# Performance work log

Measured on AMD Instinct MI355X. Metric: run time of the kernel, lower is better.

## Reference

```python
import jax, jax.numpy as jnp
import numpy as np

N, DIM = 8192, 128

def setup_inputs() -> dict:
    key = jax.random.key(0)
    ks = jax.random.split(key, 9)
    s = 1.0 / np.sqrt(DIM)
    return {
        "x": jax.random.normal(ks[0], (N, DIM), dtype=jnp.float32),
        "Wq": jax.random.uniform(ks[1], (DIM, DIM), jnp.float32, -s, s),
        "bq": jax.random.uniform(ks[2], (DIM,), jnp.float32, -s, s),
        "Wk": jax.random.uniform(ks[3], (DIM, DIM), jnp.float32, -s, s),
        "bk": jax.random.uniform(ks[4], (DIM,), jnp.float32, -s, s),
        "Wv": jax.random.uniform(ks[5], (DIM, DIM), jnp.float32, -s, s),
        "bv": jax.random.uniform(ks[6], (DIM,), jnp.float32, -s, s),
        "Wo": jax.random.uniform(ks[7], (DIM, DIM), jnp.float32, -s, s),
        "bo": jax.random.uniform(ks[8], (DIM,), jnp.float32, -s, s),
    }

def reference(x, Wq, bq, Wk, bk, Wv, bv, Wo, bo):
    # nn.Linear: y = x @ W.T + b
    Q = x @ Wq.T + bq                      # [N, d]
    K = x @ Wk.T + bk                      # [N, d]
    V = x @ Wv.T + bv                      # [N, d]
    scale = 1.0 / jnp.sqrt(jnp.asarray(x.shape[-1], x.dtype))
    scores = (Q @ K.T) * scale             # [N, N] — matches original O(n^2) math
    attn = jax.nn.softmax(scores, axis=-1)
    out = attn @ V                         # [N, d]
    return out @ Wo.T + bo
```

## Files before the change

kernel.cpp:

```cpp
#include <hip/hip_runtime.h>
#include <math.h>


typedef __bf16 bf16x8 __attribute__((ext_vector_type(8)));
typedef float f32x4 __attribute__((ext_vector_type(4)));
typedef float f32x16 __attribute__((ext_vector_type(16)));
typedef unsigned int u32x4 __attribute__((ext_vector_type(4)));
typedef unsigned int u32x2 __attribute__((ext_vector_type(2)));
typedef unsigned short us16;

#define NTOK 8192
#define CHUNKS 8

static constexpr float SCALE_L2E = 0.08838834764831845f * 1.4426950408889634f;

__device__ __forceinline__ unsigned f2bf_u(float x) {
    unsigned u = __builtin_bit_cast(unsigned, x);
    return (u + 0x7FFFu + ((u >> 16) & 1u)) >> 16;
}

__device__ __forceinline__ unsigned pk_bf16(float x, float y) {
    unsigned a = __builtin_bit_cast(unsigned, x) + 0x8000u;
    unsigned b = __builtin_bit_cast(unsigned, y) + 0x8000u;
#if __has_builtin(__builtin_amdgcn_perm)
    return __builtin_amdgcn_perm(b, a, 0x07060302u);
#else
    return (a >> 16) | (b & 0xFFFF0000u);
#endif
}

__device__ __forceinline__ bf16x8 ld_frag(const us16* p) {
    u32x4 u = *reinterpret_cast<const u32x4*>(p);
    return __builtin_bit_cast(bf16x8, u);
}

__device__ __forceinline__ bf16x8 cvt_frag(const float* p) {
    f32x4 a = *reinterpret_cast<const f32x4*>(p);
    f32x4 b = *reinterpret_cast<const f32x4*>(p + 4);
    u32x4 o;
    o[0] = f2bf_u(a[0]) | (f2bf_u(a[1]) << 16);
    o[1] = f2bf_u(a[2]) | (f2bf_u(a[3]) << 16);
    o[2] = f2bf_u(b[0]) | (f2bf_u(b[1]) << 16);
    o[3] = f2bf_u(b[2]) | (f2bf_u(b[3]) << 16);
    return __builtin_bit_cast(bf16x8, o);
}

__global__ __launch_bounds__(256) void proj_qkv(
    const float* __restrict__ x,
    const float* __restrict__ wq, const float* __restrict__ bq,
    const float* __restrict__ wk, const float* __restrict__ bk,
    const float* __restrict__ wv, const float* __restrict__ bv,
    us16* __restrict__ Qb, us16* __restrict__ Kb, us16* __restrict__ Vt)
{
    __shared__ us16 ldsT[4][16 * 136];

    int z = blockIdx.x >> 7;
    int tile = blockIdx.x & 127;
    const float* W = z == 0 ? wq : z == 1 ? wk : wv;
    const float* bias = z == 0 ? bq : z == 1 ? bk : bv;
    float osc = z == 0 ? SCALE_L2E : 1.0f;

    int w = threadIdx.x >> 6, lane = threadIdx.x & 63;
    int quad = lane >> 4, l15 = lane & 15;
    int rbase = tile * 64 + w * 16;

    bf16x8 af[4];
#pragma unroll
    for (int ks = 0; ks < 4; ++ks)
        af[ks] = cvt_frag(x + (rbase + l15) * 128 + ks * 32 + quad * 8);

    f32x4 acc[8];
#pragma unroll
    for (int nt = 0; nt < 8; ++nt) acc[nt] = f32x4{0.f, 0.f, 0.f, 0.f};

#pragma unroll
    for (int nt = 0; nt < 8; ++nt) {
#pragma unroll
        for (int ks = 0; ks < 4; ++ks) {
            bf16x8 bf = cvt_frag(W + (nt * 16 + l15) * 128 + ks * 32 + quad * 8);
            acc[nt] = __builtin_amdgcn_mfma_f32_16x16x32_bf16(af[ks], bf, acc[nt], 0, 0, 0);
        }
    }

    if (z < 2) {
        us16* T = &ldsT[w][0];
        us16* Out = z == 0 ? Qb : Kb;
#pragma unroll
        for (int nt = 0; nt < 8; ++nt) {
            float bb = bias[nt * 16 + l15];
#pragma unroll
            for (int r = 0; r < 4; ++r)
                T[(quad * 4 + r) * 136 + nt * 16 + l15] =
                    (us16)f2bf_u((acc[nt][r] + bb) * osc);
        }
        asm volatile("s_waitcnt lgkmcnt(0)" ::: "memory");
        int row = lane >> 2, seg = lane & 3;
        const us16* src = T + row * 136 + seg * 32;
        us16* dst = Out + (rbase + row) * 128 + seg * 32;
#pragma unroll
        for (int c = 0; c < 4; ++c)
            *reinterpret_cast<u32x4*>(dst + c * 8) =
                *reinterpret_cast<const u32x4*>(src + c * 8);
    } else {
#pragma unroll
        for (int nt = 0; nt < 8; ++nt) {
            float bb = bias[nt * 16 + l15];
            int d = nt * 16 + l15, r0 = rbase + quad * 4;
            u32x2 pk;
            pk[0] = f2bf_u(acc[nt][0] + bb) | (f2bf_u(acc[nt][1] + bb) << 16);
            pk[1] = f2bf_u(acc[nt][2] + bb) | (f2bf_u(acc[nt][3] + bb) << 16);
            *reinterpret_cast<u32x2*>(Vt + d * NTOK + r0) = pk;
        }
    }
}

__global__ __launch_bounds__(256, 2) void attn(
    const us16* __restrict__ Qb, const us16* __restrict__ Kb,
    const us16* __restrict__ Vt,
    float* __restrict__ Opart, float* __restrict__ Lpart)
{
    __shared__ us16 ldsK[64 * 136];
    __shared__ us16 ldsV[128 * 72];
    __shared__ us16 ldsP[4][32 * 72];

    int qtile = blockIdx.x >> 3, chunk = blockIdx.x & 7;
    int tid = threadIdx.x, w = tid >> 6, lane = tid & 63;
    int quad = lane >> 4, l15 = lane & 15;
    int qb0 = qtile * 128 + w * 32;

    bf16x8 qf[2][4];
#pragma unroll
    for (int mt = 0; mt < 2; ++mt)
#pragma unroll
        for (int ks = 0; ks < 4; ++ks)
            qf[mt][ks] = ld_frag(Qb + (qb0 + mt * 16 + l15) * 128 + ks * 32 + quad * 8);

    f32x4 o[2][8];
#pragma unroll
    for (int mt = 0; mt < 2; ++mt)
#pragma unroll
        for (int dt = 0; dt < 8; ++dt) o[mt][dt] = f32x4{0.f, 0.f, 0.f, 0.f};

    f32x4 lacc[2];
    lacc[0] = f32x4{0.f, 0.f, 0.f, 0.f};
    lacc[1] = f32x4{0.f, 0.f, 0.f, 0.f};

    u32x4 onesu;
    onesu[0] = onesu[1] = onesu[2] = onesu[3] = 0x3F803F80u;
    bf16x8 ones = __builtin_bit_cast(bf16x8, onesu);

    us16* pw = &ldsP[w][0];

    for (int it = 0; it < 16; ++it) {
        int kk = chunk * 1024 + it * 64;
#pragma unroll
        for (int c = 0; c < 4; ++c) {
            int idx = tid + c * 256;
            int r = idx >> 4, cc = idx & 15;
            *reinterpret_cast<u32x4*>(ldsK + r * 136 + cc * 8) =
                *reinterpret_cast<const u32x4*>(Kb + (kk + r) * 128 + cc * 8);
        }
#pragma unroll
        for (int c = 0; c < 4; ++c) {
            int idx = tid + c * 256;
            int r = idx >> 3, cc = idx & 7;
            *reinterpret_cast<u32x4*>(ldsV + r * 72 + cc * 8) =
                *reinterpret_cast<const u32x4*>(Vt + r * NTOK + kk + cc * 8);
        }
        __syncthreads();

        f32x4 s[2][4];
#pragma unroll
        for (int mt = 0; mt < 2; ++mt)
#pragma unroll
            for (int nt = 0; nt < 4; ++nt) s[mt][nt] = f32x4{0.f, 0.f, 0.f, 0.f};

#pragma unroll
        for (int nt = 0; nt < 4; ++nt) {
#pragma unroll
            for (int ks = 0; ks < 4; ++ks) {
                bf16x8 kf = ld_frag(ldsK + (nt * 16 + l15) * 136 + ks * 32 + quad * 8);
                s[0][nt] = __builtin_amdgcn_mfma_f32_16x16x32_bf16(kf, qf[0][ks], s[0][nt], 0, 0, 0);
                s[1][nt] = __builtin_amdgcn_mfma_f32_16x16x32_bf16(kf, qf[1][ks], s[1][nt], 0, 0, 0);
            }
        }

#pragma unroll
        for (int mt = 0; mt < 2; ++mt) {
#pragma unroll
            for (int nt = 0; nt < 4; ++nt) {
                float p0 = exp2f(s[mt][nt][0]);
                float p1 = exp2f(s[mt][nt][1]);
                float p2 = exp2f(s[mt][nt][2]);
                float p3 = exp2f(s[mt][nt][3]);
                u32x2 wv;
                wv[0] = pk_bf16(p0, p1);
                wv[1] = pk_bf16(p2, p3);
                *reinterpret_cast<u32x2*>(pw + (mt * 16 + l15) * 72 + nt * 16 + quad * 4) = wv;
            }
        }

        asm volatile("s_waitcnt lgkmcnt(0)" ::: "memory");

        bf16x8 afP[2][2];
#pragma unroll
        for (int mt = 0; mt < 2; ++mt)
#pragma unroll
            for (int k2 = 0; k2 < 2; ++k2)
                afP[mt][k2] = ld_frag(pw + (mt * 16 + l15) * 72 + k2 * 32 + quad * 8);

        lacc[0] = __builtin_amdgcn_mfma_f32_16x16x32_bf16(afP[0][0], ones, lacc[0], 0, 0, 0);
        lacc[0] = __builtin_amdgcn_mfma_f32_16x16x32_bf16(afP[0][1], ones, lacc[0], 0, 0, 0);
        lacc[1] = __builtin_amdgcn_mfma_f32_16x16x32_bf16(afP[1][0], ones, lacc[1], 0, 0, 0);
        lacc[1] = __builtin_amdgcn_mfma_f32_16x16x32_bf16(afP[1][1], ones, lacc[1], 0, 0, 0);

#pragma unroll
        for (int dt = 0; dt < 8; ++dt) {
#pragma unroll
            for (int k2 = 0; k2 < 2; ++k2) {
                bf16x8 bv = ld_frag(ldsV + (dt * 16 + l15) * 72 + k2 * 32 + quad * 8);
                o[0][dt] = __builtin_amdgcn_mfma_f32_16x16x32_bf16(afP[0][k2], bv, o[0][dt], 0, 0, 0);
                o[1][dt] = __builtin_amdgcn_mfma_f32_16x16x32_bf16(afP[1][k2], bv, o[1][dt], 0, 0, 0);
            }
        }
        __syncthreads();
    }

#pragma unroll
    for (int mt = 0; mt < 2; ++mt)
#pragma unroll
        for (int dt = 0; dt < 8; ++dt)
#pragma unroll
            for (int r = 0; r < 4; ++r) {
                int row = qb0 + mt * 16 + quad * 4 + r;
                Opart[(size_t)(chunk * NTOK + row) * 128 + dt * 16 + l15] = o[mt][dt][r];
            }
    if (l15 == 0) {
#pragma unroll
        for (int mt = 0; mt < 2; ++mt)
#pragma unroll
            for (int r = 0; r < 4; ++r) {
                int row = qb0 + mt * 16 + quad * 4 + r;
                Lpart[chunk * NTOK + row] = lacc[mt][r];
            }
    }
}

__global__ __launch_bounds__(256) void combine_proj(
    const float* __restrict__ Opart, const float* __restrict__ Lpart,
    const float* __restrict__ Wo, const float* __restrict__ bo,
    float* __restrict__ out)
{
    __shared__ us16 ldsO[32 * 136];
    __shared__ float ldsL[32];

    int tile = blockIdx.x, t = threadIdx.x;
    int r0 = tile * 32;

    if (t < 32) {
        float L = 0.f;
#pragma unroll
        for (int c = 0; c < CHUNKS; ++c) L += Lpart[c * NTOK + r0 + t];
        ldsL[t] = 1.0f / L;
    }

    f32x4 acc[4];
#pragma unroll
    for (int j = 0; j < 4; ++j) acc[j] = f32x4{0.f, 0.f, 0.f, 0.f};

#pragma unroll
    for (int c = 0; c < CHUNKS; ++c) {
        const float* src = Opart + (size_t)(c * NTOK + r0) * 128;
#pragma unroll
        for (int j = 0; j < 4; ++j) {
            f32x4 v = *reinterpret_cast<const f32x4*>(src + j * 1024 + t * 4);
            acc[j] += v;
        }
    }
    __syncthreads();

#pragma unroll
    for (int j = 0; j < 4; ++j) {
        int flat = j * 1024 + t * 4;
        int row = flat >> 7, col = flat & 127;
        float sc = ldsL[row];
        u32x2 wv;
        wv[0] = pk_bf16(acc[j][0] * sc, acc[j][1] * sc);
        wv[1] = pk_bf16(acc[j][2] * sc, acc[j][3] * sc);
        *reinterpret_cast<u32x2*>(ldsO + row * 136 + col) = wv;
    }
    __syncthreads();

    int w = t >> 6, lane = t & 63;
    int l31 = lane & 31, hi = lane >> 5;

    bf16x8 af[8];
#pragma unroll
    for (int ks = 0; ks < 8; ++ks)
        af[ks] = ld_frag(ldsO + l31 * 136 + ks * 16 + hi * 8);

    f32x16 acc2;
#pragma unroll
    for (int r = 0; r < 16; ++r) acc2[r] = 0.f;

#pragma unroll
    for (int ks = 0; ks < 8; ++ks) {
        bf16x8 bfw = cvt_frag(Wo + (w * 32 + l31) * 128 + ks * 16 + hi * 8);
        acc2 = __builtin_amdgcn_mfma_f32_32x32x16_bf16(af[ks], bfw, acc2, 0, 0, 0);
    }

    float bb = bo[w * 32 + l31];
#pragma unroll
    for (int r = 0; r < 16; ++r) {
        int m = (r & 3) + 8 * (r >> 2) + 4 * hi;
        out[(size_t)(r0 + m) * 128 + w * 32 + l31] = acc2[r] + bb;
    }
}

extern "C" void kernel_launch(void* const* d_in, const int* in_sizes, int n_in,
                              void* d_out, int out_size, void* d_ws, size_t ws_size,
                              hipStream_t stream)
{
    const float* x  = (const float*)d_in[0];
    const float* Wq = (const float*)d_in[1];
    const float* bq = (const float*)d_in[2];
    const float* Wk = (const float*)d_in[3];
    const float* bk = (const float*)d_in[4];
    const float* Wv = (const float*)d_in[5];
    const float* bv = (const float*)d_in[6];
    const float* Wo = (const float*)d_in[7];
    const float* bo = (const float*)d_in[8];

    char* ws = (char*)d_ws;
    const size_t MB = 1024 * 1024;
    us16* Qb  = (us16*)(ws + 0 * MB);
    us16* Kb  = (us16*)(ws + 2 * MB);
    us16* Vt  = (us16*)(ws + 4 * MB);
    float* Lp = (float*)(ws + 6 * MB);
    float* Op = (float*)(ws + 7 * MB);

    proj_qkv<<<384, 256, 0, stream>>>(x, Wq, bq, Wk, bk, Wv, bv, Qb, Kb, Vt);
    attn<<<512, 256, 0, stream>>>(Qb, Kb, Vt, Op, Lp);
    combine_proj<<<256, 256, 0, stream>>>(Op, Lp, Wo, bo, (float*)d_out);
}
```

Measured before the change: 153.0 us.

## Build P fragments in registers via permlane swaps instead of an LDS round-trip

The softmax probability tile is no longer written to per-wave LDS and read back. Each lane now packs bf16 pairs with the native cvt_pk instruction, and v_permlane32/16 swaps reshuffle those registers into the A-operand layout for the PV MFMA. The change also switches to the hardware exp2 builtin and wraps the MFMA loops with s_setprio so matrix work gets issue priority. The goals are to remove LDS traffic and waitcnt stalls and to shrink shared memory. The cost is correctness risk from the permlane layout mapping and the change in rounding of the bf16 conversion.

```diff
diff --git a/kernel.cpp b/kernel.cpp
--- a/kernel.cpp
+++ b/kernel.cpp
@@ -26,6 +26,28 @@
     return __builtin_amdgcn_perm(b, a, 0x07060302u);
 #else
     return (a >> 16) | (b & 0xFFFF0000u);
+#endif
+}
+
+__device__ __forceinline__ unsigned cvtpk_bf16(float x, float y) {
+    unsigned r;
+    asm("v_cvt_pk_bf16_f32 %0, %1, %2" : "=v"(r) : "v"(x), "v"(y));
+    return r;
+}
+
+__device__ __forceinline__ void plswap(unsigned& a, unsigned& b) {
+    asm("v_permlane32_swap_b32 %0, %1" : "+v"(a), "+v"(b));
+}
+
+__device__ __forceinline__ void pl16swap(unsigned& a, unsigned& b) {
+    asm("v_permlane16_swap_b32 %0, %1" : "+v"(a), "+v"(b));
+}
+
+__device__ __forceinline__ float fexp2(float x) {
+#if __has_builtin(__builtin_amdgcn_exp2f)
+    return __builtin_amdgcn_exp2f(x);
+#else
+    return exp2f(x);
 #endif
 }
 
@@ -94,6 +116,7 @@
                     (us16)f2bf_u((acc[nt][r] + bb) * osc);
         }
         asm volatile("s_waitcnt lgkmcnt(0)" ::: "memory");
+        __builtin_amdgcn_sched_barrier(0);
         int row = lane >> 2, seg = lane & 3;
         const us16* src = T + row * 136 + seg * 32;
         us16* dst = Out + (rbase + row) * 128 + seg * 32;
@@ -121,7 +144,6 @@
 {
     __shared__ us16 ldsK[64 * 136];
     __shared__ us16 ldsV[128 * 72];
-    __shared__ us16 ldsP[4][32 * 72];
 
     int qtile = blockIdx.x >> 3, chunk = blockIdx.x & 7;
     int tid = threadIdx.x, w = tid >> 6, lane = tid & 63;
@@ -148,8 +170,6 @@
     u32x4 onesu;
     onesu[0] = onesu[1] = onesu[2] = onesu[3] = 0x3F803F80u;
     bf16x8 ones = __builtin_bit_cast(bf16x8, onesu);
-
-    us16* pw = &ldsP[w][0];
 
     for (int it = 0; it < 16; ++it) {
         int kk = chunk * 1024 + it * 64;
@@ -175,6 +195,7 @@
 #pragma unroll
             for (int nt = 0; nt < 4; ++nt) s[mt][nt] = f32x4{0.f, 0.f, 0.f, 0.f};
 
+        __builtin_amdgcn_s_setprio(1);
 #pragma unroll
         for (int nt = 0; nt < 4; ++nt) {
 #pragma unroll
@@ -184,36 +205,44 @@
                 s[1][nt] = __builtin_amdgcn_mfma_f32_16x16x32_bf16(kf, qf[1][ks], s[1][nt], 0, 0, 0);
             }
         }
-
+        __builtin_amdgcn_s_setprio(0);
+
+        bf16x8 afP[2][2];
 #pragma unroll
         for (int mt = 0; mt < 2; ++mt) {
+            unsigned W[4][2];
 #pragma unroll
             for (int nt = 0; nt < 4; ++nt) {
-                float p0 = exp2f(s[mt][nt][0]);
-                float p1 = exp2f(s[mt][nt][1]);
-                float p2 = exp2f(s[mt][nt][2]);
-                float p3 = exp2f(s[mt][nt][3]);
-                u32x2 wv;
-                wv[0] = pk_bf16(p0, p1);
-                wv[1] = pk_bf16(p2, p3);
-                *reinterpret_cast<u32x2*>(pw + (mt * 16 + l15) * 72 + nt * 16 + quad * 4) = wv;
-            }
-        }
-
-        asm volatile("s_waitcnt lgkmcnt(0)" ::: "memory");
-
-        bf16x8 afP[2][2];
-#pragma unroll
-        for (int mt = 0; mt < 2; ++mt)
-#pragma unroll
-            for (int k2 = 0; k2 < 2; ++k2)
-                afP[mt][k2] = ld_frag(pw + (mt * 16 + l15) * 72 + k2 * 32 + quad * 8);
+                float p0 = fexp2(s[mt][nt][0]);
+                float p1 = fexp2(s[mt][nt][1]);
+                float p2 = fexp2(s[mt][nt][2]);
+                float p3 = fexp2(s[mt][nt][3]);
+                W[nt][0] = cvtpk_bf16(p0, p1);
+                W[nt][1] = cvtpk_bf16(p2, p3);
+            }
+#pragma unroll
+            for (int k2 = 0; k2 < 2; ++k2) {
+                u32x4 f;
+                {
+                    unsigned X = W[2 * k2][0], Y = W[2 * k2 + 1][0];
+                    plswap(X, Y); pl16swap(X, Y);
+                    f[0] = X; f[2] = Y;
+                }
+                {
+                    unsigned X = W[2 * k2][1], Y = W[2 * k2 + 1][1];
+                    plswap(X, Y); pl16swap(X, Y);
+                    f[1] = X; f[3] = Y;
+                }
+                afP[mt][k2] = __builtin_bit_cast(bf16x8, f);
+            }
+        }
 
         lacc[0] = __builtin_amdgcn_mfma_f32_16x16x32_bf16(afP[0][0], ones, lacc[0], 0, 0, 0);
         lacc[0] = __builtin_amdgcn_mfma_f32_16x16x32_bf16(afP[0][1], ones, lacc[0], 0, 0, 0);
         lacc[1] = __builtin_amdgcn_mfma_f32_16x16x32_bf16(afP[1][0], ones, lacc[1], 0, 0, 0);
         lacc[1] = __builtin_amdgcn_mfma_f32_16x16x32_bf16(afP[1][1], ones, lacc[1], 0, 0, 0);
 
+        __builtin_amdgcn_s_setprio(1);
 #pragma unroll
         for (int dt = 0; dt < 8; ++dt) {
 #pragma unroll
@@ -223,6 +252,7 @@
                 o[1][dt] = __builtin_amdgcn_mfma_f32_16x16x32_bf16(afP[1][k2], bv, o[1][dt], 0, 0, 0);
             }
         }
+        __builtin_amdgcn_s_setprio(0);
         __syncthreads();
     }
 
```

New measurement: 141.7 us. -7.4%, faster.
